# Kernel tuning notes

Measured on AMD Instinct MI355X. Metric: run time of the kernel, lower is better.

## Reference

```python
import jax, jax.numpy as jnp
import numpy as np

N = 100000
E = 1000000
P = 1000000
HID = 128
ROLE_VOCAB = 8
ROLE_DIM = 16
IDX_VOCAB = 1024
IDX_DIM = 8
FEAT = 14
IN_DIM = FEAT + IDX_DIM + ROLE_DIM  # 38


def setup_inputs() -> dict:
    key = jax.random.key(0)
    ks = jax.random.split(key, 20)
    s = 0.02
    return {
        "block_features": jax.random.normal(ks[0], (N, FEAT), jnp.float32),
        "role_ids": jax.random.randint(ks[1], (N,), 0, ROLE_VOCAB),
        "b2b_src": jax.random.randint(ks[2], (E,), 0, N),
        "b2b_dst": jax.random.randint(ks[3], (E,), 0, N),
        "b2b_w": jax.random.uniform(ks[4], (E,), jnp.float32),
        "p2b_block": jax.random.randint(ks[5], (P,), 0, N),
        "p2b_w": jax.random.uniform(ks[6], (P,), jnp.float32),
        "role_emb": jax.random.normal(ks[7], (ROLE_VOCAB, ROLE_DIM), jnp.float32),
        "idx_emb": jax.random.normal(ks[8], (IDX_VOCAB, IDX_DIM), jnp.float32),
        "W1": jax.random.normal(ks[9], (IN_DIM, HID), jnp.float32) * s,
        "b1": jnp.zeros((HID,), jnp.float32),
        "W2": jax.random.normal(ks[10], (HID, HID), jnp.float32) * s,
        "b2": jnp.zeros((HID,), jnp.float32),
        "M1": jax.random.normal(ks[11], (HID, HID), jnp.float32) * s,
        "mb1": jnp.zeros((HID,), jnp.float32),
        "M2": jax.random.normal(ks[12], (HID, HID), jnp.float32) * s,
        "mb2": jnp.zeros((HID,), jnp.float32),
        "ln_g": jnp.ones((HID,), jnp.float32),
        "ln_b": jnp.zeros((HID,), jnp.float32),
    }


def _layernorm(x, g, b, eps=1e-5):
    mu = jnp.mean(x, axis=-1, keepdims=True)
    var = jnp.mean(jnp.square(x - mu), axis=-1, keepdims=True)
    return (x - mu) * jax.lax.rsqrt(var + eps) * g + b


def reference(block_features, role_ids, b2b_src, b2b_dst, b2b_w, p2b_block, p2b_w,
              role_emb, idx_emb, W1, b1, W2, b2, M1, mb1, M2, mb2, ln_g, ln_b):
    n = block_features.shape[0]
    # embeddings + input MLP
    re = role_emb[role_ids]                                  # [N, 16]
    ie = idx_emb[jnp.arange(n) % IDX_VOCAB]                  # [N, 8]
    x = jnp.concatenate([block_features, re, ie], axis=-1)   # [N, 38]
    h = jax.nn.relu(x @ W1 + b1)
    emb = jax.nn.relu(h @ W2 + b2)                           # [N, HID]
    # b2b: symmetric weighted scatter-add of neighbor embeddings
    agg = jnp.zeros_like(emb)
    agg = agg.at[b2b_src].add(emb[b2b_dst] * b2b_w[:, None])
    agg = agg.at[b2b_dst].add(emb[b2b_src] * b2b_w[:, None])
    # p2b: agg[j] += emb[j] * w  ==  emb * (sum of pin weights per block)
    pw = jnp.zeros((n,), emb.dtype).at[p2b_block].add(p2b_w)
    agg = agg + emb * pw[:, None]
    # message MLP + residual + LayerNorm
    m = jax.nn.relu(agg @ M1 + mb1) @ M2 + mb2
    block_embeddings = _layernorm(emb + m, ln_g, ln_b)
    graph_embedding = jnp.mean(block_embeddings, axis=0)
    return block_embeddings, graph_embedding
```

## Files before the change

### kernel.cpp

```cpp
#include <hip/hip_runtime.h>

#define FEAT 14
#define ROLE_DIM 16
#define IDX_DIM 8
#define IN_DIM 38
#define HID 128
#define IDX_VOCAB 1024
#define BINN 128
#define NBINS_MAX 800
#define NSEG 1024
#define BINP_CAPT 8
#define BINP_SCAP 16
#define SORT_CAP 4096

typedef __attribute__((ext_vector_type(8))) short short8;
typedef __attribute__((ext_vector_type(4))) float f32x4;
typedef __attribute__((ext_vector_type(2))) float f32x2;

__device__ __forceinline__ ushort f2bf(float f) {
    uint u = __float_as_uint(f);
    return (ushort)((u + 0x7FFFu + ((u >> 16) & 1u)) >> 16);
}
__device__ __forceinline__ float bf2f(ushort h) {
    return __uint_as_float((uint)h << 16);
}
__device__ __forceinline__ uchar f2fp8(float f) {
    return (uchar)(__builtin_amdgcn_cvt_pk_fp8_f32(f, f, 0, false) & 0xff);
}

__global__ void k_prep(const float* __restrict__ W1, const float* __restrict__ W2,
                       const float* __restrict__ M1, const float* __restrict__ M2,
                       ushort* __restrict__ W1t, ushort* __restrict__ W2t,
                       ushort* __restrict__ M1t, ushort* __restrict__ M2t)
{
    int t = blockIdx.x * 256 + threadIdx.x;
    if (t < 8192) {
        int c = t >> 6, k = t & 63;
        W1t[t] = (k < IN_DIM) ? f2bf(W1[k * HID + c]) : (ushort)0;
    } else if (t < 24576) {
        int u = t - 8192; int c = u >> 7, k = u & 127;
        W2t[u] = f2bf(W2[k * HID + c]);
    } else if (t < 40960) {
        int u = t - 24576; int c = u >> 7, k = u & 127;
        M1t[u] = f2bf(M1[k * HID + c]);
    } else if (t < 57344) {
        int u = t - 40960; int c = u >> 7, k = u & 127;
        M2t[u] = f2bf(M2[k * HID + c]);
    }
}

#define LDSA 32768

__device__ __forceinline__ void embed_body(
    char* lds, int id,
    const float* __restrict__ feat, const int* __restrict__ role_ids,
    const float* __restrict__ role_emb, const float* __restrict__ idx_emb,
    const ushort* __restrict__ W1t, const float* __restrict__ b1,
    const ushort* __restrict__ W2t, const float* __restrict__ b2,
    ushort* __restrict__ embh, uchar* __restrict__ embf8, int N)
{
    const int tid = threadIdx.x;
    const int w = tid >> 6, l = tid & 63;
    const int li = l & 15, hi = l >> 4;
    const int base = id * 64;

    for (int c = 0; c < 4; ++c) {
        int idx = c * 256 + tid;
        int col = idx >> 3, ch = idx & 7;
        uint4 v = *(const uint4*)(W1t + col * 64 + ch * 8);
        *(uint4*)(lds + col * 256 + ((ch * 16) ^ ((col & 7) << 4))) = v;
    }
    {
        int row = tid >> 2, kq = (tid & 3) * 16;
        int gr = base + row; if (gr >= N) gr = N - 1;
        int rid = role_ids[gr];
        float xv[16];
        #pragma unroll
        for (int j = 0; j < 16; ++j) {
            int k = kq + j;
            float v = 0.0f;
            if (k < FEAT)                 v = feat[gr * FEAT + k];
            else if (k < FEAT + ROLE_DIM) v = role_emb[rid * ROLE_DIM + (k - FEAT)];
            else if (k < IN_DIM)          v = idx_emb[(gr & (IDX_VOCAB - 1)) * IDX_DIM + (k - FEAT - ROLE_DIM)];
            xv[j] = v;
        }
        uint p[8];
        #pragma unroll
        for (int j = 0; j < 8; ++j)
            p[j] = (uint)f2bf(xv[2 * j]) | ((uint)f2bf(xv[2 * j + 1]) << 16);
        char* db = lds + LDSA + row * 256;
        int sw = (row & 7) << 4;
        *(uint4*)(db + ((kq * 2) ^ sw))      = make_uint4(p[0], p[1], p[2], p[3]);
        *(uint4*)(db + ((kq * 2 + 16) ^ sw)) = make_uint4(p[4], p[5], p[6], p[7]);
    }
    __syncthreads();

    f32x4 C[8];
    #pragma unroll
    for (int ct = 0; ct < 8; ++ct) C[ct] = (f32x4){0.f, 0.f, 0.f, 0.f};
    {
        const int arow = w * 16 + li;
        const int asw = (arow & 7) << 4;
        #pragma unroll
        for (int ks = 0; ks < 2; ++ks) {
            short8 a = *(short8*)(lds + LDSA + arow * 256 + ((ks * 64 + hi * 16) ^ asw));
            #pragma unroll
            for (int ct = 0; ct < 8; ++ct) {
                int bcol = ct * 16 + li;
                short8 b = *(short8*)(lds + bcol * 256 + ((ks * 64 + hi * 16) ^ ((bcol & 7) << 4)));
                C[ct] = __builtin_amdgcn_mfma_f32_16x16x32_bf16(a, b, C[ct], 0, 0, 0);
            }
        }
    }
    __syncthreads();

    #pragma unroll
    for (int ct = 0; ct < 8; ++ct) {
        int col = ct * 16 + li;
        float bv = b1[col];
        #pragma unroll
        for (int r = 0; r < 4; ++r) {
            int hrow = w * 16 + hi * 4 + r;
            float h = fmaxf(C[ct][r] + bv, 0.0f);
            *(ushort*)(lds + LDSA + hrow * 256 + ((col * 2) ^ ((hrow & 7) << 4))) = f2bf(h);
        }
    }
    for (int c = 0; c < 8; ++c) {
        int idx = c * 256 + tid;
        int col = idx >> 4, ch = idx & 15;
        uint4 v = *(const uint4*)(W2t + col * 128 + ch * 8);
        *(uint4*)(lds + col * 256 + ((ch * 16) ^ ((col & 7) << 4))) = v;
    }
    __syncthreads();

    f32x4 C2[8];
    #pragma unroll
    for (int ct = 0; ct < 8; ++ct) C2[ct] = (f32x4){0.f, 0.f, 0.f, 0.f};
    {
        const int arow = w * 16 + li;
        const int asw = (arow & 7) << 4;
        #pragma unroll
        for (int ks = 0; ks < 4; ++ks) {
            short8 a = *(short8*)(lds + LDSA + arow * 256 + ((ks * 64 + hi * 16) ^ asw));
            #pragma unroll
            for (int ct = 0; ct < 8; ++ct) {
                int bcol = ct * 16 + li;
                short8 b = *(short8*)(lds + bcol * 256 + ((ks * 64 + hi * 16) ^ ((bcol & 7) << 4)));
                C2[ct] = __builtin_amdgcn_mfma_f32_16x16x32_bf16(a, b, C2[ct], 0, 0, 0);
            }
        }
    }

    #pragma unroll
    for (int ct = 0; ct < 8; ++ct) {
        int col = ct * 16 + li;
        float bv = b2[col];
        #pragma unroll
        for (int r = 0; r < 4; ++r) {
            int gr = base + w * 16 + hi * 4 + r;
            if (gr < N) {
                float o = fmaxf(C2[ct][r] + bv, 0.0f);
                embh[(size_t)gr * 128 + col] = f2bf(o);
                embf8[(size_t)gr * 128 + col] = f2fp8(o);
            }
        }
    }
}

__device__ __forceinline__ void binp_body(
    char* lds, int id,
    const int* __restrict__ src, const int* __restrict__ dst,
    const float* __restrict__ wgt, uint* __restrict__ staged,
    int* __restrict__ cnt,
    const int* __restrict__ pb, const float* __restrict__ pv,
    float* __restrict__ pw,
    int E, int P, int nbins, int chunkE, int chunkP)
{
    uint* buf   = (uint*)lds;
    int* curT   = (int*)(lds + 25600);
    int* segCur = (int*)(lds + 28800);
    const int tid = threadIdx.x;
    for (int i = tid; i < nbins; i += 256) { curT[i] = 0; segCur[i] = 0; }
    __syncthreads();

    const int lo = id * chunkE;
    const int hiE = (lo + chunkE) < E ? (lo + chunkE) : E;
    for (int i = lo + tid; i < hiE; i += 256) {
        int s = src[i], d = dst[i];
        uint q = (uint)(wgt[i] * 255.0f + 0.5f);
        int bs = s >> 7;
        uint es = ((uint)(s & 127) << 25) | ((uint)d << 8) | q;
        int ps = atomicAdd(&curT[bs], 1);
        if (ps < BINP_CAPT) buf[bs * BINP_CAPT + ps] = es;
        else if (ps < BINP_SCAP)
            staged[((size_t)bs * NSEG + id) * BINP_SCAP + ps] = es;
        int bd = d >> 7;
        uint ed = ((uint)(d & 127) << 25) | ((uint)s << 8) | q;
        int pd = atomicAdd(&curT[bd], 1);
        if (pd < BINP_CAPT) buf[bd * BINP_CAPT + pd] = ed;
        else if (pd < BINP_SCAP)
            staged[((size_t)bd * NSEG + id) * BINP_SCAP + pd] = ed;
    }
    __syncthreads();
    for (int b = tid; b < nbins; b += 256) {
        int tot = curT[b];
        int k = tot < BINP_CAPT ? tot : BINP_CAPT;
        uint* dp = staged + ((size_t)b * NSEG + id) * BINP_SCAP;
        for (int i = 0; i < k; ++i) dp[i] = buf[b * BINP_CAPT + i];
        cnt[id * nbins + b] = tot < BINP_SCAP ? tot : BINP_SCAP;
    }

    int loP = id * chunkP;
    int hiP = loP + chunkP; if (hiP > P) hiP = P;
    for (int i = loP + tid; i < hiP; i += 256)
        atomicAdd(&pw[pb[i]], pv[i]);
}

__global__ __launch_bounds__(256) void k_embed_binp(
    const float* __restrict__ feat, const int* __restrict__ role_ids,
    const float* __restrict__ role_emb, const float* __restrict__ idx_emb,
    const ushort* __restrict__ W1t, const float* __restrict__ b1,
    const ushort* __restrict__ W2t, const float* __restrict__ b2,
    ushort* __restrict__ embh, uchar* __restrict__ embf8,
    const int* __restrict__ src, const int* __restrict__ dst,
    const float* __restrict__ wgt, uint* __restrict__ staged,
    int* __restrict__ cnt,
    const int* __restrict__ pb, const float* __restrict__ pv,
    float* __restrict__ pw,
    int N, int E, int P, int nbins, int chunkE, int chunkP)
{
    __shared__ char lds[49152];
    const int bid = blockIdx.x;
    int role, id;
    if (bid < 2 * NSEG) { role = bid & 1; id = bid >> 1; }
    else                { role = 0; id = NSEG + (bid - 2 * NSEG); }

    if (role == 0)
        embed_body(lds, id, feat, role_ids, role_emb, idx_emb,
                   W1t, b1, W2t, b2, embh, embf8, N);
    else
        binp_body(lds, id, src, dst, wgt, staged, cnt, pb, pv, pw,
                  E, P, nbins, chunkE, chunkP);
}

#define AREG 32768
#define WSUM 65536

__global__ __launch_bounds__(256) void k_agg_mlp(
    const uint* __restrict__ staged, const int* __restrict__ cnt,
    const ushort* __restrict__ embh, const uchar* __restrict__ embf8,
    const float* __restrict__ pw,
    const ushort* __restrict__ M1t, const ushort* __restrict__ M2t,
    const float* __restrict__ mb1, const float* __restrict__ mb2,
    const float* __restrict__ ln_g, const float* __restrict__ ln_b,
    float* __restrict__ out, float* __restrict__ gsum, int N, int nbins)
{
    __shared__ char lds[67584];
    uint* sorted  = (uint*)lds;
    int*  hist    = (int*)(lds + 16384);
    int*  startL  = (int*)(lds + 16384 + 512);
    int*  curL    = (int*)(lds + 16384 + 1024);
    int*  sc      = (int*)(lds + 16384 + 1536);

    const int tid = threadIdx.x;
    const int b = blockIdx.x;
    const int baseNode = b << 7;
    const int w = tid >> 6, l = tid & 63;
    const int li = l & 15, hi = l >> 4;

    if (tid < BINN) hist[tid] = 0;
    __syncthreads();

    int cSeg[4];
    #pragma unroll
    for (int ss = 0; ss < 4; ++ss) {
        int seg = ss * 256 + tid;
        cSeg[ss] = cnt[seg * nbins + b];
        const uint* sp = staged + ((size_t)b * NSEG + seg) * BINP_SCAP;
        for (int k = 0; k < cSeg[ss]; ++k)
            atomicAdd(&hist[sp[k] >> 25], 1);
    }
    __syncthreads();

    int v = (tid < BINN) ? hist[tid] : 0;
    if (tid < BINN) sc[tid] = v;
    __syncthreads();
    for (int off = 1; off < BINN; off <<= 1) {
        int u = (tid < BINN && tid >= off) ? sc[tid - off] : 0;
        __syncthreads();
        if (tid < BINN) sc[tid] += u;
        __syncthreads();
    }
    if (tid < BINN) {
        startL[tid] = sc[tid] - v;
        curL[tid]   = sc[tid] - v;
    }
    __syncthreads();

    #pragma unroll
    for (int ss = 0; ss < 4; ++ss) {
        int seg = ss * 256 + tid;
        const uint* sp = staged + ((size_t)b * NSEG + seg) * BINP_SCAP;
        for (int k = 0; k < cSeg[ss]; ++k) {
            uint e = sp[k];
            int pos = atomicAdd(&curL[e >> 25], 1);
            if (pos < SORT_CAP) sorted[pos] = e;
        }
    }
    __syncthreads();

    {
        const int g  = tid >> 3;
        const int cg = tid & 7;
        const int c0 = cg * 16;
        for (int h = 0; h < 4; ++h) {
            int nl = h * 32 + g;
            int node = baseNode + nl;
            uint p[8];
            if (node < N) {
                float acc[16];
                float pwn = pw[node];
                const uint4* r = (const uint4*)(embh + ((size_t)node << 7) + c0);
                uint4 u0 = r[0], u1 = r[1];
                uint uu[8] = {u0.x, u0.y, u0.z, u0.w, u1.x, u1.y, u1.z, u1.w};
                #pragma unroll
                for (int j = 0; j < 8; ++j) {
                    acc[2*j]   = __uint_as_float(uu[j] << 16) * pwn;
                    acc[2*j+1] = __uint_as_float(uu[j] & 0xffff0000u) * pwn;
                }
                const int st = startL[nl], deg = hist[nl];
                #pragma unroll 4
                for (int i = 0; i < deg; ++i) {
                    uint en = sorted[st + i];
                    int nb   = (int)((en >> 8) & 0x1FFFFu);
                    float wt = (float)(en & 255u) * (1.0f / 255.0f);
                    uint4 q = *(const uint4*)(embf8 + ((size_t)nb << 7) + c0);
                    uint qq[4] = {q.x, q.y, q.z, q.w};
                    #pragma unroll
                    for (int j = 0; j < 4; ++j) {
                        f32x2 lo = __builtin_amdgcn_cvt_pk_f32_fp8(qq[j], false);
                        f32x2 hi2 = __builtin_amdgcn_cvt_pk_f32_fp8(qq[j], true);
                        acc[4*j+0] = fmaf(lo.x,  wt, acc[4*j+0]);
                        acc[4*j+1] = fmaf(lo.y,  wt, acc[4*j+1]);
                        acc[4*j+2] = fmaf(hi2.x, wt, acc[4*j+2]);
                        acc[4*j+3] = fmaf(hi2.y, wt, acc[4*j+3]);
                    }
                }
                #pragma unroll
                for (int j = 0; j < 8; ++j)
                    p[j] = (uint)f2bf(acc[2*j]) | ((uint)f2bf(acc[2*j+1]) << 16);
            } else {
                #pragma unroll
                for (int j = 0; j < 8; ++j) p[j] = 0;
            }
            char* db = lds + AREG + nl * 256;
            int sw = (nl & 7) << 4;
            *(uint4*)(db + ((c0 * 2) ^ sw))      = make_uint4(p[0], p[1], p[2], p[3]);
            *(uint4*)(db + ((c0 * 2 + 16) ^ sw)) = make_uint4(p[4], p[5], p[6], p[7]);
        }
    }
    __syncthreads();

    for (int cc = 0; cc < 8; ++cc) {
        int idx = cc * 256 + tid;
        int col = idx >> 4, ch = idx & 15;
        uint4 vv = *(const uint4*)(M1t + col * 128 + ch * 8);
        *(uint4*)(lds + col * 256 + ((ch * 16) ^ ((col & 7) << 4))) = vv;
    }
    __syncthreads();

    #pragma unroll
    for (int h2 = 0; h2 < 2; ++h2) {
        f32x4 C1[8];
        #pragma unroll
        for (int ct = 0; ct < 8; ++ct) C1[ct] = (f32x4){0.f, 0.f, 0.f, 0.f};
        const int arow = h2 * 64 + w * 16 + li;
        const int asw = (arow & 7) << 4;
        #pragma unroll
        for (int ks = 0; ks < 4; ++ks) {
            short8 a = *(short8*)(lds + AREG + arow * 256 + ((ks * 64 + hi * 16) ^ asw));
            #pragma unroll
            for (int ct = 0; ct < 8; ++ct) {
                int bcol = ct * 16 + li;
                short8 bb = *(short8*)(lds + bcol * 256 + ((ks * 64 + hi * 16) ^ ((bcol & 7) << 4)));
                C1[ct] = __builtin_amdgcn_mfma_f32_16x16x32_bf16(a, bb, C1[ct], 0, 0, 0);
            }
        }
        #pragma unroll
        for (int ct = 0; ct < 8; ++ct) {
            int col = ct * 16 + li;
            float bv = mb1[col];
            #pragma unroll
            for (int r = 0; r < 4; ++r) {
                int hrow = h2 * 64 + w * 16 + hi * 4 + r;
                float h = fmaxf(C1[ct][r] + bv, 0.0f);
                *(ushort*)(lds + AREG + hrow * 256 + ((col * 2) ^ ((hrow & 7) << 4))) = f2bf(h);
            }
        }
    }
    __syncthreads();

    for (int cc = 0; cc < 8; ++cc) {
        int idx = cc * 256 + tid;
        int col = idx >> 4, ch = idx & 15;
        uint4 vv = *(const uint4*)(M2t + col * 128 + ch * 8);
        *(uint4*)(lds + col * 256 + ((ch * 16) ^ ((col & 7) << 4))) = vv;
    }
    __syncthreads();

    float cs[8];
    #pragma unroll
    for (int ct = 0; ct < 8; ++ct) cs[ct] = 0.0f;

    #pragma unroll
    for (int h2 = 0; h2 < 2; ++h2) {
        f32x4 C2[8];
        #pragma unroll
        for (int ct = 0; ct < 8; ++ct) C2[ct] = (f32x4){0.f, 0.f, 0.f, 0.f};
        const int arow = h2 * 64 + w * 16 + li;
        const int asw = (arow & 7) << 4;
        #pragma unroll
        for (int ks = 0; ks < 4; ++ks) {
            short8 a = *(short8*)(lds + AREG + arow * 256 + ((ks * 64 + hi * 16) ^ asw));
            #pragma unroll
            for (int ct = 0; ct < 8; ++ct) {
                int bcol = ct * 16 + li;
                short8 bb = *(short8*)(lds + bcol * 256 + ((ks * 64 + hi * 16) ^ ((bcol & 7) << 4)));
                C2[ct] = __builtin_amdgcn_mfma_f32_16x16x32_bf16(a, bb, C2[ct], 0, 0, 0);
            }
        }

        float y[8][4];
        #pragma unroll
        for (int ct = 0; ct < 8; ++ct) {
            int col = ct * 16 + li;
            float bv = mb2[col];
            #pragma unroll
            for (int r = 0; r < 4; ++r) {
                int gr = baseNode + h2 * 64 + w * 16 + hi * 4 + r;
                int grc = gr < N ? gr : N - 1;
                y[ct][r] = C2[ct][r] + bv + bf2f(embh[(size_t)grc * 128 + col]);
            }
        }
        float rs[4] = {0, 0, 0, 0}, rq[4] = {0, 0, 0, 0};
        #pragma unroll
        for (int ct = 0; ct < 8; ++ct)
            #pragma unroll
            for (int r = 0; r < 4; ++r) { rs[r] += y[ct][r]; rq[r] += y[ct][r] * y[ct][r]; }
        #pragma unroll
        for (int m = 1; m < 16; m <<= 1) {
            #pragma unroll
            for (int r = 0; r < 4; ++r) {
                rs[r] += __shfl_xor(rs[r], m);
                rq[r] += __shfl_xor(rq[r], m);
            }
        }
        float mu[4], rstd[4];
        #pragma unroll
        for (int r = 0; r < 4; ++r) {
            mu[r] = rs[r] * (1.0f / HID);
            float var = rq[r] * (1.0f / HID) - mu[r] * mu[r];
            rstd[r] = rsqrtf(var + 1e-5f);
        }
        #pragma unroll
        for (int ct = 0; ct < 8; ++ct) {
            int col = ct * 16 + li;
            float g = ln_g[col], bb2 = ln_b[col];
            #pragma unroll
            for (int r = 0; r < 4; ++r) {
                int gr = baseNode + h2 * 64 + w * 16 + hi * 4 + r;
                float o = (y[ct][r] - mu[r]) * rstd[r] * g + bb2;
                if (gr < N) {
                    out[(size_t)gr * 128 + col] = o;
                    cs[ct] += o;
                }
            }
        }
    }

    #pragma unroll
    for (int m = 16; m < 64; m <<= 1) {
        #pragma unroll
        for (int ct = 0; ct < 8; ++ct) cs[ct] += __shfl_xor(cs[ct], m);
    }
    float* wsum = (float*)(lds + WSUM);
    if (hi == 0) {
        #pragma unroll
        for (int ct = 0; ct < 8; ++ct) wsum[w * 128 + ct * 16 + li] = cs[ct];
    }
    __syncthreads();
    if (tid < 128) {
        float s = wsum[tid] + wsum[128 + tid] + wsum[256 + tid] + wsum[384 + tid];
        atomicAdd(&gsum[tid], s);
    }
}

__global__ void k_graph(const float* __restrict__ gsum, float* __restrict__ out,
                        int N)
{
    int j = threadIdx.x;
    out[(size_t)N * HID + j] = gsum[j] * (1.0f / (float)N);
}

extern "C" void kernel_launch(void* const* d_in, const int* in_sizes, int n_in,
                              void* d_out, int out_size, void* d_ws, size_t ws_size,
                              hipStream_t stream)
{
    const float* feat      = (const float*)d_in[0];
    const int*   role_ids  = (const int*)  d_in[1];
    const int*   b2b_src   = (const int*)  d_in[2];
    const int*   b2b_dst   = (const int*)  d_in[3];
    const float* b2b_w     = (const float*)d_in[4];
    const int*   p2b_block = (const int*)  d_in[5];
    const float* p2b_w     = (const float*)d_in[6];
    const float* role_emb  = (const float*)d_in[7];
    const float* idx_emb   = (const float*)d_in[8];
    const float* W1        = (const float*)d_in[9];
    const float* b1        = (const float*)d_in[10];
    const float* W2        = (const float*)d_in[11];
    const float* b2        = (const float*)d_in[12];
    const float* M1        = (const float*)d_in[13];
    const float* mb1       = (const float*)d_in[14];
    const float* M2        = (const float*)d_in[15];
    const float* mb2       = (const float*)d_in[16];
    const float* ln_g      = (const float*)d_in[17];
    const float* ln_b      = (const float*)d_in[18];

    const int N = in_sizes[1];
    const int E = in_sizes[2];
    const int P = in_sizes[5];

    float* out = (float*)d_out;

    const int nbins = (N + BINN - 1) >> 7;
    const int chunkE = (E + NSEG - 1) / NSEG;
    const int chunkP = (P + NSEG - 1) / NSEG;

    char* ws = (char*)d_ws;
    size_t embhBytes = (size_t)N * HID * sizeof(ushort);
    size_t embf8Bytes= (size_t)N * HID;
    size_t stagBytes = (size_t)nbins * NSEG * BINP_SCAP * sizeof(uint);
    size_t cntBytes  = (((size_t)NSEG * nbins * sizeof(int)) + 15) & ~15ull;
    size_t vecBytes  = (size_t)N * sizeof(float);

    ushort* embh    = (ushort*)ws;  ws += embhBytes;
    uchar*  embf8   = (uchar*)ws;   ws += embf8Bytes;
    uint*   staged  = (uint*)ws;    ws += stagBytes;
    int*    cnt     = (int*)ws;     ws += cntBytes;
    float*  pw      = (float*)ws;   ws += vecBytes;
    float*  gsum    = (float*)ws;   ws += 512;
    ushort* W1t     = (ushort*)ws;  ws += 8192  * sizeof(ushort);
    ushort* W2t     = (ushort*)ws;  ws += 16384 * sizeof(ushort);
    ushort* M1t     = (ushort*)ws;  ws += 16384 * sizeof(ushort);
    ushort* M2t     = (ushort*)ws;  ws += 16384 * sizeof(ushort);

    hipMemsetAsync(pw, 0, vecBytes + 512, stream);

    const int nEmbed = (N + 63) / 64;

    k_prep<<<224, 256, 0, stream>>>(W1, W2, M1, M2, W1t, W2t, M1t, M2t);

    k_embed_binp<<<nEmbed + NSEG, 256, 0, stream>>>(
        feat, role_ids, role_emb, idx_emb, W1t, b1, W2t, b2, embh, embf8,
        b2b_src, b2b_dst, b2b_w, staged, cnt, p2b_block, p2b_w, pw,
        N, E, P, nbins, chunkE, chunkP);

    k_agg_mlp<<<nbins, 256, 0, stream>>>(
        staged, cnt, embh, embf8, pw, M1t, M2t, mb1, mb2, ln_g, ln_b,
        out, gsum, N, nbins);

    k_graph<<<1, HID, 0, stream>>>(gsum, out, N);
}
```

Measured before the change: 217.6 us.

## Split fused aggregation+MLP kernel into separate gather and message/LayerNorm kernels

The single per-bin kernel that gathered neighbour embeddings and then ran the two message-MLP matmuls and LayerNorm is split in two. k_agg now only does the sorted gather with a small LDS footprint and writes the bf16 aggregate to a new global buffer. A separate k_msg_ln kernel processes 64-row tiles and does the MFMA matmuls, residual, LayerNorm and graph-sum reduction. The aim is higher occupancy for the latency-bound gather phase, at the cost of an extra global write and read of the N×128 bf16 aggregate plus one more kernel launch.

```diff
diff --git a/kernel.cpp b/kernel.cpp
--- a/kernel.cpp
+++ b/kernel.cpp
@@ -178,9 +178,8 @@
 {
     uint* buf   = (uint*)lds;
     int* curT   = (int*)(lds + 25600);
-    int* segCur = (int*)(lds + 28800);
     const int tid = threadIdx.x;
-    for (int i = tid; i < nbins; i += 256) { curT[i] = 0; segCur[i] = 0; }
+    for (int i = tid; i < nbins; i += 256) curT[i] = 0;
     __syncthreads();
 
     const int lo = id * chunkE;
@@ -243,30 +242,21 @@
                   E, P, nbins, chunkE, chunkP);
 }
 
-#define AREG 32768
-#define WSUM 65536
-
-__global__ __launch_bounds__(256) void k_agg_mlp(
+__global__ __launch_bounds__(256) void k_agg(
     const uint* __restrict__ staged, const int* __restrict__ cnt,
     const ushort* __restrict__ embh, const uchar* __restrict__ embf8,
     const float* __restrict__ pw,
-    const ushort* __restrict__ M1t, const ushort* __restrict__ M2t,
-    const float* __restrict__ mb1, const float* __restrict__ mb2,
-    const float* __restrict__ ln_g, const float* __restrict__ ln_b,
-    float* __restrict__ out, float* __restrict__ gsum, int N, int nbins)
-{
-    __shared__ char lds[67584];
-    uint* sorted  = (uint*)lds;
-    int*  hist    = (int*)(lds + 16384);
-    int*  startL  = (int*)(lds + 16384 + 512);
-    int*  curL    = (int*)(lds + 16384 + 1024);
-    int*  sc      = (int*)(lds + 16384 + 1536);
+    ushort* __restrict__ aggh, int N, int nbins)
+{
+    __shared__ int hist[BINN];
+    __shared__ int startL[BINN];
+    __shared__ int curL[BINN];
+    __shared__ int sc[BINN];
+    __shared__ uint sorted[SORT_CAP];
 
     const int tid = threadIdx.x;
     const int b = blockIdx.x;
     const int baseNode = b << 7;
-    const int w = tid >> 6, l = tid & 63;
-    const int li = l & 15, hi = l >> 4;
 
     if (tid < BINN) hist[tid] = 0;
     __syncthreads();
@@ -309,181 +299,192 @@
     }
     __syncthreads();
 
+    const int g  = tid >> 3;
+    const int cg = tid & 7;
+    const int c0 = cg * 16;
+    for (int h = 0; h < 4; ++h) {
+        int nl = h * 32 + g;
+        int node = baseNode + nl;
+        if (node < N) {
+            float acc[16];
+            float pwn = pw[node];
+            const uint4* r = (const uint4*)(embh + ((size_t)node << 7) + c0);
+            uint4 u0 = r[0], u1 = r[1];
+            uint uu[8] = {u0.x, u0.y, u0.z, u0.w, u1.x, u1.y, u1.z, u1.w};
+            #pragma unroll
+            for (int j = 0; j < 8; ++j) {
+                acc[2*j]   = __uint_as_float(uu[j] << 16) * pwn;
+                acc[2*j+1] = __uint_as_float(uu[j] & 0xffff0000u) * pwn;
+            }
+            const int st = startL[nl], deg = hist[nl];
+            #pragma unroll 4
+            for (int i = 0; i < deg; ++i) {
+                uint en = sorted[st + i];
+                int nb   = (int)((en >> 8) & 0x1FFFFu);
+                float wt = (float)(en & 255u) * (1.0f / 255.0f);
+                uint4 q = *(const uint4*)(embf8 + ((size_t)nb << 7) + c0);
+                uint qq[4] = {q.x, q.y, q.z, q.w};
+                #pragma unroll
+                for (int j = 0; j < 4; ++j) {
+                    f32x2 lo = __builtin_amdgcn_cvt_pk_f32_fp8(qq[j], false);
+                    f32x2 hi2 = __builtin_amdgcn_cvt_pk_f32_fp8(qq[j], true);
+                    acc[4*j+0] = fmaf(lo.x,  wt, acc[4*j+0]);
+                    acc[4*j+1] = fmaf(lo.y,  wt, acc[4*j+1]);
+                    acc[4*j+2] = fmaf(hi2.x, wt, acc[4*j+2]);
+                    acc[4*j+3] = fmaf(hi2.y, wt, acc[4*j+3]);
+                }
+            }
+            uint p[8];
+            #pragma unroll
+            for (int j = 0; j < 8; ++j)
+                p[j] = (uint)f2bf(acc[2*j]) | ((uint)f2bf(acc[2*j+1]) << 16);
+            uint4* ap = (uint4*)(aggh + ((size_t)node << 7) + c0);
+            ap[0] = make_uint4(p[0], p[1], p[2], p[3]);
+            ap[1] = make_uint4(p[4], p[5], p[6], p[7]);
+        }
+    }
+}
+
+#define LDSS 49152
+
+__global__ __launch_bounds__(256) void k_msg_ln(
+    const ushort* __restrict__ aggh, const ushort* __restrict__ embh,
+    const ushort* __restrict__ M1t, const ushort* __restrict__ M2t,
+    const float* __restrict__ mb1, const float* __restrict__ mb2,
+    const float* __restrict__ ln_g, const float* __restrict__ ln_b,
+    float* __restrict__ out, float* __restrict__ gsum, int N)
+{
+    __shared__ char lds[51200];
+    const int tid = threadIdx.x;
+    const int w = tid >> 6, l = tid & 63;
+    const int li = l & 15, hi = l >> 4;
+    const int base = blockIdx.x * 64;
+
+    for (int c = 0; c < 8; ++c) {
+        int idx = c * 256 + tid;
+        int col = idx >> 4, ch = idx & 15;
+        uint4 v = *(const uint4*)(M1t + col * 128 + ch * 8);
+        *(uint4*)(lds + col * 256 + ((ch * 16) ^ ((col & 7) << 4))) = v;
+    }
+    for (int c = 0; c < 4; ++c) {
+        int idx = c * 256 + tid;
+        int row = idx >> 4, ch = idx & 15;
+        int gr = base + row; if (gr >= N) gr = N - 1;
+        uint4 v = *(const uint4*)(aggh + (size_t)gr * 128 + ch * 8);
+        *(uint4*)(lds + LDSA + row * 256 + ((ch * 16) ^ ((row & 7) << 4))) = v;
+    }
+    __syncthreads();
+
+    f32x4 C[8];
+    #pragma unroll
+    for (int ct = 0; ct < 8; ++ct) C[ct] = (f32x4){0.f, 0.f, 0.f, 0.f};
     {
-        const int g  = tid >> 3;
-        const int cg = tid & 7;
-        const int c0 = cg * 16;
-        for (int h = 0; h < 4; ++h) {
-            int nl = h * 32 + g;
-            int node = baseNode + nl;
-            uint p[8];
-            if (node < N) {
-                float acc[16];
-                float pwn = pw[node];
-                const uint4* r = (const uint4*)(embh + ((size_t)node << 7) + c0);
-                uint4 u0 = r[0], u1 = r[1];
-                uint uu[8] = {u0.x, u0.y, u0.z, u0.w, u1.x, u1.y, u1.z, u1.w};
-                #pragma unroll
-                for (int j = 0; j < 8; ++j) {
-                    acc[2*j]   = __uint_as_float(uu[j] << 16) * pwn;
-                    acc[2*j+1] = __uint_as_float(uu[j] & 0xffff0000u) * pwn;
-                }
-                const int st = startL[nl], deg = hist[nl];
-                #pragma unroll 4
-                for (int i = 0; i < deg; ++i) {
-                    uint en = sorted[st + i];
-                    int nb   = (int)((en >> 8) & 0x1FFFFu);
-                    float wt = (float)(en & 255u) * (1.0f / 255.0f);
-                    uint4 q = *(const uint4*)(embf8 + ((size_t)nb << 7) + c0);
-                    uint qq[4] = {q.x, q.y, q.z, q.w};
-                    #pragma unroll
-                    for (int j = 0; j < 4; ++j) {
-                        f32x2 lo = __builtin_amdgcn_cvt_pk_f32_fp8(qq[j], false);
-                        f32x2 hi2 = __builtin_amdgcn_cvt_pk_f32_fp8(qq[j], true);
-                        acc[4*j+0] = fmaf(lo.x,  wt, acc[4*j+0]);
-                        acc[4*j+1] = fmaf(lo.y,  wt, acc[4*j+1]);
-                        acc[4*j+2] = fmaf(hi2.x, wt, acc[4*j+2]);
-                        acc[4*j+3] = fmaf(hi2.y, wt, acc[4*j+3]);
-                    }
-                }
-                #pragma unroll
-                for (int j = 0; j < 8; ++j)
-                    p[j] = (uint)f2bf(acc[2*j]) | ((uint)f2bf(acc[2*j+1]) << 16);
-            } else {
-                #pragma unroll
-                for (int j = 0; j < 8; ++j) p[j] = 0;
-            }
-            char* db = lds + AREG + nl * 256;
-            int sw = (nl & 7) << 4;
-            *(uint4*)(db + ((c0 * 2) ^ sw))      = make_uint4(p[0], p[1], p[2], p[3]);
-            *(uint4*)(db + ((c0 * 2 + 16) ^ sw)) = make_uint4(p[4], p[5], p[6], p[7]);
-        }
-    }
-    __syncthreads();
-
-    for (int cc = 0; cc < 8; ++cc) {
-        int idx = cc * 256 + tid;
-        int col = idx >> 4, ch = idx & 15;
-        uint4 vv = *(const uint4*)(M1t + col * 128 + ch * 8);
-        *(uint4*)(lds + col * 256 + ((ch * 16) ^ ((col & 7) << 4))) = vv;
-    }
-    __syncthreads();
-
-    #pragma unroll
-    for (int h2 = 0; h2 < 2; ++h2) {
-        f32x4 C1[8];
-        #pragma unroll
-        for (int ct = 0; ct < 8; ++ct) C1[ct] = (f32x4){0.f, 0.f, 0.f, 0.f};
-        const int arow = h2 * 64 + w * 16 + li;
+        const int arow = w * 16 + li;
         const int asw = (arow & 7) << 4;
         #pragma unroll
         for (int ks = 0; ks < 4; ++ks) {
-            short8 a = *(short8*)(lds + AREG + arow * 256 + ((ks * 64 + hi * 16) ^ asw));
+            short8 a = *(short8*)(lds + LDSA + arow * 256 + ((ks * 64 + hi * 16) ^ asw));
             #pragma unroll
             for (int ct = 0; ct < 8; ++ct) {
                 int bcol = ct * 16 + li;
-                short8 bb = *(short8*)(lds + bcol * 256 + ((ks * 64 + hi * 16) ^ ((bcol & 7) << 4)));
-                C1[ct] = __builtin_amdgcn_mfma_f32_16x16x32_bf16(a, bb, C1[ct], 0, 0, 0);
-            }
-        }
-        #pragma unroll
-        for (int ct = 0; ct < 8; ++ct) {
-            int col = ct * 16 + li;
-            float bv = mb1[col];
-            #pragma unroll
-            for (int r = 0; r < 4; ++r) {
-                int hrow = h2 * 64 + w * 16 + hi * 4 + r;
-                float h = fmaxf(C1[ct][r] + bv, 0.0f);
-                *(ushort*)(lds + AREG + hrow * 256 + ((col * 2) ^ ((hrow & 7) << 4))) = f2bf(h);
-            }
-        }
-    }
-    __syncthreads();
-
-    for (int cc = 0; cc < 8; ++cc) {
-        int idx = cc * 256 + tid;
+                short8 b = *(short8*)(lds + bcol * 256 + ((ks * 64 + hi * 16) ^ ((bcol & 7) << 4)));
+                C[ct] = __builtin_amdgcn_mfma_f32_16x16x32_bf16(a, b, C[ct], 0, 0, 0);
+            }
+        }
+    }
+    __syncthreads();
+
+    #pragma unroll
+    for (int ct = 0; ct < 8; ++ct) {
+        int col = ct * 16 + li;
+        float bv = mb1[col];
+        #pragma unroll
+        for (int r = 0; r < 4; ++r) {
+            int hrow = w * 16 + hi * 4 + r;
+            float h = fmaxf(C[ct][r] + bv, 0.0f);
+            *(ushort*)(lds + LDSA + hrow * 256 + ((col * 2) ^ ((hrow & 7) << 4))) = f2bf(h);
+        }
+    }
+    for (int c = 0; c < 8; ++c) {
+        int idx = c * 256 + tid;
         int col = idx >> 4, ch = idx & 15;
-        uint4 vv = *(const uint4*)(M2t + col * 128 + ch * 8);
-        *(uint4*)(lds + col * 256 + ((ch * 16) ^ ((col & 7) << 4))) = vv;
-    }
-    __syncthreads();
-
-    float cs[8];
-    #pragma unroll
-    for (int ct = 0; ct < 8; ++ct) cs[ct] = 0.0f;
-
-    #pragma unroll
-    for (int h2 = 0; h2 < 2; ++h2) {
-        f32x4 C2[8];
-        #pragma unroll
-        for (int ct = 0; ct < 8; ++ct) C2[ct] = (f32x4){0.f, 0.f, 0.f, 0.f};
-        const int arow = h2 * 64 + w * 16 + li;
+        uint4 v = *(const uint4*)(M2t + col * 128 + ch * 8);
+        *(uint4*)(lds + col * 256 + ((ch * 16) ^ ((col & 7) << 4))) = v;
+    }
+    __syncthreads();
+
+    f32x4 C2[8];
+    #pragma unroll
+    for (int ct = 0; ct < 8; ++ct) C2[ct] = (f32x4){0.f, 0.f, 0.f, 0.f};
+    {
+        const int arow = w * 16 + li;
         const int asw = (arow & 7) << 4;
         #pragma unroll
         for (int ks = 0; ks < 4; ++ks) {
-            short8 a = *(short8*)(lds + AREG + arow * 256 + ((ks * 64 + hi * 16) ^ asw));
+            short8 a = *(short8*)(lds + LDSA + arow * 256 + ((ks * 64 + hi * 16) ^ asw));
             #pragma unroll
             for (int ct = 0; ct < 8; ++ct) {
                 int bcol = ct * 16 + li;
-                short8 bb = *(short8*)(lds + bcol * 256 + ((ks * 64 + hi * 16) ^ ((bcol & 7) << 4)));
-                C2[ct] = __builtin_amdgcn_mfma_f32_16x16x32_bf16(a, bb, C2[ct], 0, 0, 0);
-            }
-        }
-
-        float y[8][4];
-        #pragma unroll
-        for (int ct = 0; ct < 8; ++ct) {
-            int col = ct * 16 + li;
-            float bv = mb2[col];
-            #pragma unroll
-            for (int r = 0; r < 4; ++r) {
-                int gr = baseNode + h2 * 64 + w * 16 + hi * 4 + r;
-                int grc = gr < N ? gr : N - 1;
-                y[ct][r] = C2[ct][r] + bv + bf2f(embh[(size_t)grc * 128 + col]);
-            }
-        }
-        float rs[4] = {0, 0, 0, 0}, rq[4] = {0, 0, 0, 0};
-        #pragma unroll
-        for (int ct = 0; ct < 8; ++ct)
-            #pragma unroll
-            for (int r = 0; r < 4; ++r) { rs[r] += y[ct][r]; rq[r] += y[ct][r] * y[ct][r]; }
-        #pragma unroll
-        for (int m = 1; m < 16; m <<= 1) {
-            #pragma unroll
-            for (int r = 0; r < 4; ++r) {
-                rs[r] += __shfl_xor(rs[r], m);
-                rq[r] += __shfl_xor(rq[r], m);
-            }
-        }
-        float mu[4], rstd[4];
+                short8 b = *(short8*)(lds + bcol * 256 + ((ks * 64 + hi * 16) ^ ((bcol & 7) << 4)));
+                C2[ct] = __builtin_amdgcn_mfma_f32_16x16x32_bf16(a, b, C2[ct], 0, 0, 0);
+            }
+        }
+    }
+
+    float y[8][4];
+    #pragma unroll
+    for (int ct = 0; ct < 8; ++ct) {
+        int col = ct * 16 + li;
+        float bv = mb2[col];
         #pragma unroll
         for (int r = 0; r < 4; ++r) {
-            mu[r] = rs[r] * (1.0f / HID);
-            float var = rq[r] * (1.0f / HID) - mu[r] * mu[r];
-            rstd[r] = rsqrtf(var + 1e-5f);
-        }
-        #pragma unroll
-        for (int ct = 0; ct < 8; ++ct) {
-            int col = ct * 16 + li;
-            float g = ln_g[col], bb2 = ln_b[col];
-            #pragma unroll
-            for (int r = 0; r < 4; ++r) {
-                int gr = baseNode + h2 * 64 + w * 16 + hi * 4 + r;
-                float o = (y[ct][r] - mu[r]) * rstd[r] * g + bb2;
-                if (gr < N) {
-                    out[(size_t)gr * 128 + col] = o;
-                    cs[ct] += o;
-                }
-            }
-        }
-    }
-
+            int gr = base + w * 16 + hi * 4 + r;
+            int grc = gr < N ? gr : N - 1;
+            y[ct][r] = C2[ct][r] + bv + bf2f(embh[(size_t)grc * 128 + col]);
+        }
+    }
+    float rs[4] = {0, 0, 0, 0}, rq[4] = {0, 0, 0, 0};
+    #pragma unroll
+    for (int ct = 0; ct < 8; ++ct)
+        #pragma unroll
+        for (int r = 0; r < 4; ++r) { rs[r] += y[ct][r]; rq[r] += y[ct][r] * y[ct][r]; }
+    #pragma unroll
+    for (int m = 1; m < 16; m <<= 1) {
+        #pragma unroll
+        for (int r = 0; r < 4; ++r) {
+            rs[r] += __shfl_xor(rs[r], m);
+            rq[r] += __shfl_xor(rq[r], m);
+        }
+    }
+    float mu[4], rstd[4];
+    #pragma unroll
+    for (int r = 0; r < 4; ++r) {
+        mu[r] = rs[r] * (1.0f / HID);
+        float var = rq[r] * (1.0f / HID) - mu[r] * mu[r];
+        rstd[r] = rsqrtf(var + 1e-5f);
+    }
+    float cs[8];
+    #pragma unroll
+    for (int ct = 0; ct < 8; ++ct) {
+        cs[ct] = 0.0f;
+        int col = ct * 16 + li;
+        float g = ln_g[col], bb = ln_b[col];
+        #pragma unroll
+        for (int r = 0; r < 4; ++r) {
+            int gr = base + w * 16 + hi * 4 + r;
+            float o = (y[ct][r] - mu[r]) * rstd[r] * g + bb;
+            if (gr < N) {
+                out[(size_t)gr * 128 + col] = o;
+                cs[ct] += o;
+            }
+        }
+    }
     #pragma unroll
     for (int m = 16; m < 64; m <<= 1) {
         #pragma unroll
         for (int ct = 0; ct < 8; ++ct) cs[ct] += __shfl_xor(cs[ct], m);
     }
-    float* wsum = (float*)(lds + WSUM);
+    float* wsum = (float*)(lds + LDSS);
     if (hi == 0) {
         #pragma unroll
         for (int ct = 0; ct < 8; ++ct) wsum[w * 128 + ct * 16 + li] = cs[ct];
@@ -544,6 +545,7 @@
     size_t vecBytes  = (size_t)N * sizeof(float);
 
     ushort* embh    = (ushort*)ws;  ws += embhBytes;
+    ushort* aggh    = (ushort*)ws;  ws += embhBytes;
     uchar*  embf8   = (uchar*)ws;   ws += embf8Bytes;
     uint*   staged  = (uint*)ws;    ws += stagBytes;
     int*    cnt     = (int*)ws;     ws += cntBytes;
@@ -565,9 +567,11 @@
         b2b_src, b2b_dst, b2b_w, staged, cnt, p2b_block, p2b_w, pw,
         N, E, P, nbins, chunkE, chunkP);
 
-    k_agg_mlp<<<nbins, 256, 0, stream>>>(
-        staged, cnt, embh, embf8, pw, M1t, M2t, mb1, mb2, ln_g, ln_b,
-        out, gsum, N, nbins);
+    k_agg<<<nbins, 256, 0, stream>>>(staged, cnt, embh, embf8, pw, aggh,
+                                     N, nbins);
+
+    k_msg_ln<<<(N + 63) / 64, 256, 0, stream>>>(
+        aggh, embh, M1t, M2t, mb1, mb2, ln_g, ln_b, out, gsum, N);
 
     k_graph<<<1, HID, 0, stream>>>(gsum, out, N);
 }
```

Measured after the change: 222.3 us. 2.2% more time.
